# Kernel optimization log

Measured on AMD Instinct MI355X. Metric: run time of the kernel, lower is better.

The kernel has to match this reference:

```python
import jax, jax.numpy as jnp
import numpy as np

MARGIN = 0.3
N, D = 8192, 128
NUM_CLASSES = 512


def setup_inputs() -> dict:
    key = jax.random.key(0)
    k1, k2 = jax.random.split(key)
    embeddings = jax.random.normal(k1, (N, D), dtype=jnp.float32)
    targets = jax.random.randint(k2, (N,), 0, NUM_CLASSES, dtype=jnp.int64)
    return {"embeddings": embeddings, "targets": targets}


def reference(embeddings, targets):
    x = embeddings.astype(jnp.float32)
    # pairwise squared-euclidean: ||xi||^2 + ||xj||^2 - 2 xi.xj, clamped then sqrt
    sq = jnp.sum(x * x, axis=1)  # [N]
    dist = sq[:, None] + sq[None, :] - 2.0 * (x @ x.T)
    dist = jnp.sqrt(jnp.clip(dist, 1e-12, None))  # [N, N]

    is_pos = targets[:, None] == targets[None, :]  # includes diagonal, as in torch code

    # batch-hard mining: per-row hardest positive (max) and hardest negative (min)
    dist_ap = jnp.max(jnp.where(is_pos, dist, -jnp.inf), axis=1)
    dist_an = jnp.min(jnp.where(is_pos, jnp.inf, dist), axis=1)

    # MarginRankingLoss(margin)(dist_an, dist_ap, y=1) = mean(relu(margin - (dist_an - dist_ap)))
    loss = jnp.mean(jax.nn.relu(dist_ap - dist_an + MARGIN))
    return loss
```

## Files before the change

### kernel.cpp

```cpp
#include <hip/hip_runtime.h>
#include <hip/hip_bf16.h>

#define N_ROWS 8192
#define DIM 128
#define MARGIN_F 0.3f

typedef __attribute__((ext_vector_type(8))) short short8;
typedef __attribute__((ext_vector_type(4))) float f32x4;
typedef __attribute__((ext_vector_type(4))) int int4v;

__global__ __launch_bounds__(256) void prep_kernel(
    const float* __restrict__ x, const int* __restrict__ tgt,
    unsigned short* __restrict__ xbA, unsigned short* __restrict__ xbB,
    float2* __restrict__ meta, int* __restrict__ apb, int* __restrict__ anb) {
  const int w = threadIdx.x >> 6, l = threadIdx.x & 63;
  const int row = blockIdx.x * 4 + w;
  float2 v = reinterpret_cast<const float2*>(x + (size_t)row * DIM)[l];
  __hip_bfloat16 b0 = __float2bfloat16(v.x);
  __hip_bfloat16 b1 = __float2bfloat16(v.y);
  __hip_bfloat16 a0 = __float2bfloat16(-2.f * v.x);
  __hip_bfloat16 a1 = __float2bfloat16(-2.f * v.y);
  ushort2 stB, stA;
  stB.x = *reinterpret_cast<unsigned short*>(&b0);
  stB.y = *reinterpret_cast<unsigned short*>(&b1);
  stA.x = *reinterpret_cast<unsigned short*>(&a0);
  stA.y = *reinterpret_cast<unsigned short*>(&a1);
  const int c16 = row >> 4, l15r = row & 15;
  const int unit = c16 * 256 + (l >> 4) * 64 + ((l >> 2) & 3) * 16 + l15r;
  reinterpret_cast<ushort2*>(xbB)[unit * 4 + (l & 3)] = stB;
  reinterpret_cast<ushort2*>(xbA)[unit * 4 + (l & 3)] = stA;

  float s = v.x * v.x + v.y * v.y;
  #pragma unroll
  for (int off = 32; off >= 1; off >>= 1) s += __shfl_xor(s, off);
  if (l == 0) {
    float2 m;
    m.x = s;
    m.y = __int_as_float(tgt[row]);
    meta[row] = m;
    apb[row] = 0x00000000;
    anb[row] = 0x7f800000;
  }
}

__global__ __launch_bounds__(256, 2) void gram_mine_kernel(
    const unsigned short* __restrict__ xbA, const unsigned short* __restrict__ xbB,
    const float2* __restrict__ meta, int* __restrict__ apb, int* __restrict__ anb) {
  const int t = threadIdx.x;
  const int w = t >> 6, l = t & 63;
  const int l15 = l & 15, l4 = l >> 4;
  const int rb = blockIdx.x * 128 + w * 32;
  const int chunk = blockIdx.y * 1024;
  const int chunkb = chunk >> 4;

  const short8* xfA = reinterpret_cast<const short8*>(xbA);
  const short8* xfB = reinterpret_cast<const short8*>(xbB);

  short8 a0[4], a1[4];
  #pragma unroll
  for (int kk = 0; kk < 4; ++kk) {
    a0[kk] = xfA[(rb >> 4) * 256 + kk * 64 + l];
    a1[kk] = xfA[((rb >> 4) + 1) * 256 + kk * 64 + l];
  }

  int t_r[8];
  #pragma unroll
  for (int rf = 0; rf < 2; ++rf)
    #pragma unroll
    for (int rg = 0; rg < 4; ++rg)
      t_r[rf * 4 + rg] = __float_as_int(meta[rb + rf * 16 + l4 * 4 + rg].y);

  float ap2[8], an2[8];
  #pragma unroll
  for (int i = 0; i < 8; ++i) { ap2[i] = -__builtin_inff(); an2[i] = __builtin_inff(); }

  short8 bb0[8], bb1[8];
  float2 mc0[2], mc1[2];
  f32x4 accA[2][2], accB[2][2];

#define PREF_B(IDX, BB) do {                                                  \
    const int cb16_ = chunkb + (IDX) * 2;                                     \
    _Pragma("unroll")                                                         \
    for (int kk_ = 0; kk_ < 4; ++kk_) {                                       \
      BB[kk_ * 2 + 0] = xfB[(cb16_ + 0) * 256 + kk_ * 64 + l];                \
      BB[kk_ * 2 + 1] = xfB[(cb16_ + 1) * 256 + kk_ * 64 + l];                \
    } } while (0)

#define META_L(IDX, MC) do {                                                  \
    MC[0] = meta[chunk + (IDX) * 32 + l15];                                   \
    MC[1] = meta[chunk + (IDX) * 32 + 16 + l15];  } while (0)

#define MFMA_T(BB, MC, ACC) do {                                              \
    _Pragma("unroll")                                                         \
    for (int cf_ = 0; cf_ < 2; ++cf_) {                                       \
      float s_ = MC[cf_].x;                                                   \
      f32x4 ci_ = {s_, s_, s_, s_};                                           \
      ACC[0][cf_] = ci_; ACC[1][cf_] = ci_;                                   \
    }                                                                         \
    _Pragma("unroll")                                                         \
    for (int kk_ = 0; kk_ < 4; ++kk_) {                                       \
      _Pragma("unroll")                                                       \
      for (int cf_ = 0; cf_ < 2; ++cf_) {                                     \
        ACC[0][cf_] = __builtin_amdgcn_mfma_f32_16x16x32_bf16(                \
            a0[kk_], BB[kk_ * 2 + cf_], ACC[0][cf_], 0, 0, 0);                \
        ACC[1][cf_] = __builtin_amdgcn_mfma_f32_16x16x32_bf16(                \
            a1[kk_], BB[kk_ * 2 + cf_], ACC[1][cf_], 0, 0, 0);                \
      } } } while (0)

#define EPI_T(ACC, MC) do {                                                   \
    _Pragma("unroll")                                                         \
    for (int cf_ = 0; cf_ < 2; ++cf_) {                                       \
      const int tc_ = __float_as_int(MC[cf_].y);                              \
      _Pragma("unroll")                                                       \
      for (int rf_ = 0; rf_ < 2; ++rf_) {                                     \
        _Pragma("unroll")                                                     \
        for (int rg_ = 0; rg_ < 4; ++rg_) {                                   \
          const int ix_ = rf_ * 4 + rg_;                                      \
          float v_ = ACC[rf_][cf_][rg_];                                      \
          bool p_ = (t_r[ix_] == tc_);                                        \
          ap2[ix_] = p_ ? fmaxf(ap2[ix_], v_) : ap2[ix_];                     \
          an2[ix_] = p_ ? an2[ix_] : fminf(an2[ix_], v_);                     \
        } } } } while (0)

  PREF_B(0, bb0); META_L(0, mc0);
  MFMA_T(bb0, mc0, accA); PREF_B(1, bb1); META_L(1, mc1);

  #pragma unroll 1
  for (int p = 0; p < 15; ++p) {
    const int o = 2 * p + 1;
    MFMA_T(bb1, mc1, accB); PREF_B(o + 1, bb0); EPI_T(accA, mc0); META_L(o + 1, mc0);
    MFMA_T(bb0, mc0, accA); PREF_B(o + 2, bb1); EPI_T(accB, mc1); META_L(o + 2, mc1);
  }
  MFMA_T(bb1, mc1, accB); EPI_T(accA, mc0); EPI_T(accB, mc1);

#undef PREF_B
#undef META_L
#undef MFMA_T
#undef EPI_T

  #pragma unroll
  for (int i = 0; i < 8; ++i) {
    #pragma unroll
    for (int off = 1; off < 16; off <<= 1) {
      ap2[i] = fmaxf(ap2[i], __shfl_xor(ap2[i], off));
      an2[i] = fminf(an2[i], __shfl_xor(an2[i], off));
    }
  }
  if (l15 == 0) {
    #pragma unroll
    for (int rf = 0; rf < 2; ++rf)
      #pragma unroll
      for (int rg = 0; rg < 4; ++rg) {
        int row = rb + rf * 16 + l4 * 4 + rg;
        float sqr = meta[row].x;
        float a2 = fmaxf(ap2[rf * 4 + rg] + sqr, 1e-12f);
        float n2 = fmaxf(an2[rf * 4 + rg] + sqr, 1e-12f);
        atomicMax(apb + row, __float_as_int(a2));
        atomicMin(anb + row, __float_as_int(n2));
      }
  }
}

__global__ __launch_bounds__(1024) void loss_kernel(
    const int4v* __restrict__ apb, const int4v* __restrict__ anb,
    float* __restrict__ out) {
  __shared__ float red[16];
  float s = 0.f;
  for (int i = threadIdx.x; i < N_ROWS / 4; i += 1024) {
    int4v a4 = apb[i], n4 = anb[i];
    #pragma unroll
    for (int j = 0; j < 4; ++j) {
      float ap = sqrtf(__int_as_float(a4[j]));
      float an = sqrtf(__int_as_float(n4[j]));
      float li = ap - an + MARGIN_F;
      s += li > 0.f ? li : 0.f;
    }
  }
  #pragma unroll
  for (int off = 32; off >= 1; off >>= 1) s += __shfl_xor(s, off);
  const int w = threadIdx.x >> 6, l = threadIdx.x & 63;
  if (l == 0) red[w] = s;
  __syncthreads();
  if (threadIdx.x < 16) {
    float v = red[threadIdx.x];
    #pragma unroll
    for (int off = 8; off >= 1; off >>= 1) v += __shfl_xor(v, off);
    if (threadIdx.x == 0) out[0] = v / (float)N_ROWS;
  }
}

extern "C" void kernel_launch(void* const* d_in, const int* in_sizes, int n_in,
                              void* d_out, int out_size, void* d_ws, size_t ws_size,
                              hipStream_t stream) {
  const float* x = (const float*)d_in[0];
  const int* tgt = (const int*)d_in[1];
  float* out = (float*)d_out;

  char* ws = (char*)d_ws;
  unsigned short* xbA = (unsigned short*)ws;
  unsigned short* xbB = (unsigned short*)(ws + 2097152);
  float2* meta = (float2*)(ws + 4194304);
  int* apb = (int*)(ws + 4194304 + 65536);
  int* anb = (int*)(ws + 4194304 + 65536 + 32768);

  prep_kernel<<<2048, 256, 0, stream>>>(x, tgt, xbA, xbB, meta, apb, anb);
  gram_mine_kernel<<<dim3(64, 8), 256, 0, stream>>>(xbA, xbB, meta, apb, anb);
  loss_kernel<<<1, 1024, 0, stream>>>((const int4v*)apb, (const int4v*)anb, out);
}
```

Measured before the change: 44.28 us.

## Sort rows by class to skip positive-mask checks on disjoint tiles

Adds histogram and scatter kernels that counting-sort rows by target class. Embeddings are then laid out in class order, and each tile checks whether its row and column class ranges overlap. Tiles with disjoint ranges use a cheap min-only epilogue and skip the per-element class compare and max/min selects. This costs two extra kernel launches, one of which is a single-block scan, plus indirect row gathers and scattered atomics.

```diff
diff --git a/kernel.cpp b/kernel.cpp
--- a/kernel.cpp
+++ b/kernel.cpp
@@ -3,19 +3,54 @@
 
 #define N_ROWS 8192
 #define DIM 128
+#define NUM_CLS 512
 #define MARGIN_F 0.3f
 
 typedef __attribute__((ext_vector_type(8))) short short8;
 typedef __attribute__((ext_vector_type(4))) float f32x4;
 typedef __attribute__((ext_vector_type(4))) int int4v;
 
+__global__ __launch_bounds__(512) void hist_kernel(
+    const int* __restrict__ tgt, int* __restrict__ class_start,
+    int* __restrict__ cnt) {
+  __shared__ int h[NUM_CLS];
+  const int t = threadIdx.x;
+  h[t] = 0;
+  cnt[t] = 0;
+  __syncthreads();
+  for (int i = t; i < N_ROWS; i += 512) atomicAdd(&h[tgt[i]], 1);
+  __syncthreads();
+  int own = h[t];
+  int incl = own;
+  for (int off = 1; off < NUM_CLS; off <<= 1) {
+    int v = (t >= off) ? h[t - off] : 0;
+    __syncthreads();
+    incl += v;
+    h[t] = incl;
+    __syncthreads();
+  }
+  class_start[t] = incl - own;
+}
+
+__global__ __launch_bounds__(256) void scatter_kernel(
+    const int* __restrict__ tgt, const int* __restrict__ class_start,
+    int* __restrict__ cnt, int* __restrict__ sorted_row, int* __restrict__ cls) {
+  const int i = blockIdx.x * 256 + threadIdx.x;
+  const int c = tgt[i];
+  const int pos = class_start[c] + atomicAdd(&cnt[c], 1);
+  sorted_row[pos] = i;
+  cls[pos] = c;
+}
+
 __global__ __launch_bounds__(256) void prep_kernel(
-    const float* __restrict__ x, const int* __restrict__ tgt,
-    unsigned short* __restrict__ xbA, unsigned short* __restrict__ xbB,
-    float2* __restrict__ meta, int* __restrict__ apb, int* __restrict__ anb) {
+    const float* __restrict__ x, const int* __restrict__ sorted_row,
+    const int* __restrict__ cls, unsigned short* __restrict__ xbA,
+    unsigned short* __restrict__ xbB, float2* __restrict__ meta,
+    int* __restrict__ apb, int* __restrict__ anb) {
   const int w = threadIdx.x >> 6, l = threadIdx.x & 63;
-  const int row = blockIdx.x * 4 + w;
-  float2 v = reinterpret_cast<const float2*>(x + (size_t)row * DIM)[l];
+  const int j = blockIdx.x * 4 + w;
+  const int r = sorted_row[j];
+  float2 v = reinterpret_cast<const float2*>(x + (size_t)r * DIM)[l];
   __hip_bfloat16 b0 = __float2bfloat16(v.x);
   __hip_bfloat16 b1 = __float2bfloat16(v.y);
   __hip_bfloat16 a0 = __float2bfloat16(-2.f * v.x);
@@ -25,7 +60,7 @@
   stB.y = *reinterpret_cast<unsigned short*>(&b1);
   stA.x = *reinterpret_cast<unsigned short*>(&a0);
   stA.y = *reinterpret_cast<unsigned short*>(&a1);
-  const int c16 = row >> 4, l15r = row & 15;
+  const int c16 = j >> 4, l15r = j & 15;
   const int unit = c16 * 256 + (l >> 4) * 64 + ((l >> 2) & 3) * 16 + l15r;
   reinterpret_cast<ushort2*>(xbB)[unit * 4 + (l & 3)] = stB;
   reinterpret_cast<ushort2*>(xbA)[unit * 4 + (l & 3)] = stA;
@@ -36,16 +71,17 @@
   if (l == 0) {
     float2 m;
     m.x = s;
-    m.y = __int_as_float(tgt[row]);
-    meta[row] = m;
-    apb[row] = 0x00000000;
-    anb[row] = 0x7f800000;
+    m.y = __int_as_float(cls[j]);
+    meta[j] = m;
+    apb[r] = 0x00000000;
+    anb[r] = 0x7f800000;
   }
 }
 
 __global__ __launch_bounds__(256, 2) void gram_mine_kernel(
     const unsigned short* __restrict__ xbA, const unsigned short* __restrict__ xbB,
-    const float2* __restrict__ meta, int* __restrict__ apb, int* __restrict__ anb) {
+    const float2* __restrict__ meta, const int* __restrict__ cls,
+    const int* __restrict__ sorted_row, int* __restrict__ apb, int* __restrict__ anb) {
   const int t = threadIdx.x;
   const int w = t >> 6, l = t & 63;
   const int l15 = l & 15, l4 = l >> 4;
@@ -63,6 +99,7 @@
     a1[kk] = xfA[((rb >> 4) + 1) * 256 + kk * 64 + l];
   }
 
+  const int rcl_lo = cls[rb], rcl_hi = cls[rb + 31];
   int t_r[8];
   #pragma unroll
   for (int rf = 0; rf < 2; ++rf)
@@ -76,6 +113,7 @@
 
   short8 bb0[8], bb1[8];
   float2 mc0[2], mc1[2];
+  int cl0a, cl0b, cl1a, cl1b;
   f32x4 accA[2][2], accB[2][2];
 
 #define PREF_B(IDX, BB) do {                                                  \
@@ -86,9 +124,11 @@
       BB[kk_ * 2 + 1] = xfB[(cb16_ + 1) * 256 + kk_ * 64 + l];                \
     } } while (0)
 
-#define META_L(IDX, MC) do {                                                  \
+#define META_L(IDX, MC, CLA, CLB) do {                                        \
     MC[0] = meta[chunk + (IDX) * 32 + l15];                                   \
-    MC[1] = meta[chunk + (IDX) * 32 + 16 + l15];  } while (0)
+    MC[1] = meta[chunk + (IDX) * 32 + 16 + l15];                              \
+    CLA = cls[chunk + (IDX) * 32];                                            \
+    CLB = cls[chunk + (IDX) * 32 + 31]; } while (0)
 
 #define MFMA_T(BB, MC, ACC) do {                                              \
     _Pragma("unroll")                                                         \
@@ -107,31 +147,47 @@
             a1[kk_], BB[kk_ * 2 + cf_], ACC[1][cf_], 0, 0, 0);                \
       } } } while (0)
 
-#define EPI_T(ACC, MC) do {                                                   \
-    _Pragma("unroll")                                                         \
-    for (int cf_ = 0; cf_ < 2; ++cf_) {                                       \
-      const int tc_ = __float_as_int(MC[cf_].y);                              \
+#define EPI_T(ACC, MC, CLA, CLB) do {                                         \
+    if ((CLB) < rcl_lo || (CLA) > rcl_hi) {                                   \
+                               \
       _Pragma("unroll")                                                       \
       for (int rf_ = 0; rf_ < 2; ++rf_) {                                     \
         _Pragma("unroll")                                                     \
         for (int rg_ = 0; rg_ < 4; ++rg_) {                                   \
           const int ix_ = rf_ * 4 + rg_;                                      \
-          float v_ = ACC[rf_][cf_][rg_];                                      \
-          bool p_ = (t_r[ix_] == tc_);                                        \
-          ap2[ix_] = p_ ? fmaxf(ap2[ix_], v_) : ap2[ix_];                     \
-          an2[ix_] = p_ ? an2[ix_] : fminf(an2[ix_], v_);                     \
-        } } } } while (0)
-
-  PREF_B(0, bb0); META_L(0, mc0);
-  MFMA_T(bb0, mc0, accA); PREF_B(1, bb1); META_L(1, mc1);
+          an2[ix_] = fminf(fminf(ACC[rf_][0][rg_], ACC[rf_][1][rg_]),         \
+                           an2[ix_]);                                         \
+        } }                                                                   \
+    } else {                                                                  \
+      _Pragma("unroll")                                                       \
+      for (int cf_ = 0; cf_ < 2; ++cf_) {                                     \
+        const int tc_ = __float_as_int(MC[cf_].y);                            \
+        _Pragma("unroll")                                                     \
+        for (int rf_ = 0; rf_ < 2; ++rf_) {                                   \
+          _Pragma("unroll")                                                   \
+          for (int rg_ = 0; rg_ < 4; ++rg_) {                                 \
+            const int ix_ = rf_ * 4 + rg_;                                    \
+            float v_ = ACC[rf_][cf_][rg_];                                    \
+            bool p_ = (t_r[ix_] == tc_);                                      \
+            ap2[ix_] = p_ ? fmaxf(ap2[ix_], v_) : ap2[ix_];                   \
+            an2[ix_] = p_ ? an2[ix_] : fminf(an2[ix_], v_);                   \
+          } } }                                                               \
+    } } while (0)
+
+  PREF_B(0, bb0); META_L(0, mc0, cl0a, cl0b);
+  MFMA_T(bb0, mc0, accA); PREF_B(1, bb1); META_L(1, mc1, cl1a, cl1b);
 
   #pragma unroll 1
   for (int p = 0; p < 15; ++p) {
     const int o = 2 * p + 1;
-    MFMA_T(bb1, mc1, accB); PREF_B(o + 1, bb0); EPI_T(accA, mc0); META_L(o + 1, mc0);
-    MFMA_T(bb0, mc0, accA); PREF_B(o + 2, bb1); EPI_T(accB, mc1); META_L(o + 2, mc1);
-  }
-  MFMA_T(bb1, mc1, accB); EPI_T(accA, mc0); EPI_T(accB, mc1);
+    MFMA_T(bb1, mc1, accB); PREF_B(o + 1, bb0);
+    EPI_T(accA, mc0, cl0a, cl0b); META_L(o + 1, mc0, cl0a, cl0b);
+    MFMA_T(bb0, mc0, accA); PREF_B(o + 2, bb1);
+    EPI_T(accB, mc1, cl1a, cl1b); META_L(o + 2, mc1, cl1a, cl1b);
+  }
+  MFMA_T(bb1, mc1, accB);
+  EPI_T(accA, mc0, cl0a, cl0b);
+  EPI_T(accB, mc1, cl1a, cl1b);
 
 #undef PREF_B
 #undef META_L
@@ -152,11 +208,12 @@
       #pragma unroll
       for (int rg = 0; rg < 4; ++rg) {
         int row = rb + rf * 16 + l4 * 4 + rg;
+        int ro = sorted_row[row];
         float sqr = meta[row].x;
         float a2 = fmaxf(ap2[rf * 4 + rg] + sqr, 1e-12f);
         float n2 = fmaxf(an2[rf * 4 + rg] + sqr, 1e-12f);
-        atomicMax(apb + row, __float_as_int(a2));
-        atomicMin(anb + row, __float_as_int(n2));
+        atomicMax(apb + ro, __float_as_int(a2));
+        atomicMin(anb + ro, __float_as_int(n2));
       }
   }
 }
@@ -200,10 +257,17 @@
   unsigned short* xbA = (unsigned short*)ws;
   unsigned short* xbB = (unsigned short*)(ws + 2097152);
   float2* meta = (float2*)(ws + 4194304);
-  int* apb = (int*)(ws + 4194304 + 65536);
-  int* anb = (int*)(ws + 4194304 + 65536 + 32768);
-
-  prep_kernel<<<2048, 256, 0, stream>>>(x, tgt, xbA, xbB, meta, apb, anb);
-  gram_mine_kernel<<<dim3(64, 8), 256, 0, stream>>>(xbA, xbB, meta, apb, anb);
+  int* apb = (int*)(ws + 4259840);
+  int* anb = (int*)(ws + 4292608);
+  int* sorted_row = (int*)(ws + 4325376);
+  int* cls = (int*)(ws + 4358144);
+  int* class_start = (int*)(ws + 4390912);
+  int* cnt = (int*)(ws + 4392960);
+
+  hist_kernel<<<1, 512, 0, stream>>>(tgt, class_start, cnt);
+  scatter_kernel<<<32, 256, 0, stream>>>(tgt, class_start, cnt, sorted_row, cls);
+  prep_kernel<<<2048, 256, 0, stream>>>(x, sorted_row, cls, xbA, xbB, meta, apb, anb);
+  gram_mine_kernel<<<dim3(64, 8), 256, 0, stream>>>(xbA, xbB, meta, cls,
+                                                    sorted_row, apb, anb);
   loss_kernel<<<1, 1024, 0, stream>>>((const int4v*)apb, (const int4v*)anb, out);
 }
```

Measured after the change: 50.67 us. 14.4% more time.

## Stage B tiles in LDS via async global_load_lds with XOR swizzle

Applied to the files above, without the earlier changes.

Before, every wave fetched B fragments straight from global memory into registers. Now B is stored row-major by the prep kernel, and each block cooperatively stages 64-column slices into a 4-buffer LDS ring using direct global-to-LDS loads, with an XOR swizzle to avoid bank conflicts. Blocks grow to 512 threads (8 waves) sharing each B tile, and the grid changes to 32x16. This cuts redundant global and L2 traffic for B, at the cost of barriers per slice, 64KB of LDS per block, and a smaller in-register accumulator pipeline.

```diff
diff --git a/kernel.cpp b/kernel.cpp
--- a/kernel.cpp
+++ b/kernel.cpp
@@ -9,9 +9,16 @@
 typedef __attribute__((ext_vector_type(4))) float f32x4;
 typedef __attribute__((ext_vector_type(4))) int int4v;
 
+typedef const void __attribute__((address_space(1)))* gas1_t;
+typedef void __attribute__((address_space(3)))* las3_t;
+
+__device__ __forceinline__ void load_lds16(const void* g, void* l) {
+  __builtin_amdgcn_global_load_lds((gas1_t)g, (las3_t)l, 16, 0, 0);
+}
+
 __global__ __launch_bounds__(256) void prep_kernel(
     const float* __restrict__ x, const int* __restrict__ tgt,
-    unsigned short* __restrict__ xbA, unsigned short* __restrict__ xbB,
+    unsigned short* __restrict__ xbA, unsigned short* __restrict__ xbBrow,
     float2* __restrict__ meta, int* __restrict__ apb, int* __restrict__ anb) {
   const int w = threadIdx.x >> 6, l = threadIdx.x & 63;
   const int row = blockIdx.x * 4 + w;
@@ -25,9 +32,9 @@
   stB.y = *reinterpret_cast<unsigned short*>(&b1);
   stA.x = *reinterpret_cast<unsigned short*>(&a0);
   stA.y = *reinterpret_cast<unsigned short*>(&a1);
+  reinterpret_cast<ushort2*>(xbBrow)[(size_t)row * 64 + l] = stB;
   const int c16 = row >> 4, l15r = row & 15;
   const int unit = c16 * 256 + (l >> 4) * 64 + ((l >> 2) & 3) * 16 + l15r;
-  reinterpret_cast<ushort2*>(xbB)[unit * 4 + (l & 3)] = stB;
   reinterpret_cast<ushort2*>(xbA)[unit * 4 + (l & 3)] = stA;
 
   float s = v.x * v.x + v.y * v.y;
@@ -43,18 +50,18 @@
   }
 }
 
-__global__ __launch_bounds__(256, 2) void gram_mine_kernel(
-    const unsigned short* __restrict__ xbA, const unsigned short* __restrict__ xbB,
+__global__ __launch_bounds__(512, 4) void gram_mine_kernel(
+    const unsigned short* __restrict__ xbA, const unsigned short* __restrict__ xbBrow,
     const float2* __restrict__ meta, int* __restrict__ apb, int* __restrict__ anb) {
+  __shared__ unsigned short Bs[4][64 * 128];
+
   const int t = threadIdx.x;
   const int w = t >> 6, l = t & 63;
   const int l15 = l & 15, l4 = l >> 4;
-  const int rb = blockIdx.x * 128 + w * 32;
-  const int chunk = blockIdx.y * 1024;
-  const int chunkb = chunk >> 4;
+  const int rb = blockIdx.x * 256 + w * 32;
+  const int chunk = blockIdx.y * 512;
 
   const short8* xfA = reinterpret_cast<const short8*>(xbA);
-  const short8* xfB = reinterpret_cast<const short8*>(xbB);
 
   short8 a0[4], a1[4];
   #pragma unroll
@@ -74,69 +81,77 @@
   #pragma unroll
   for (int i = 0; i < 8; ++i) { ap2[i] = -__builtin_inff(); an2[i] = __builtin_inff(); }
 
-  short8 bb0[8], bb1[8];
-  float2 mc0[2], mc1[2];
-  f32x4 accA[2][2], accB[2][2];
-
-#define PREF_B(IDX, BB) do {                                                  \
-    const int cb16_ = chunkb + (IDX) * 2;                                     \
-    _Pragma("unroll")                                                         \
-    for (int kk_ = 0; kk_ < 4; ++kk_) {                                       \
-      BB[kk_ * 2 + 0] = xfB[(cb16_ + 0) * 256 + kk_ * 64 + l];                \
-      BB[kk_ * 2 + 1] = xfB[(cb16_ + 1) * 256 + kk_ * 64 + l];                \
+#define STAGE(BUF, S) do {                                                    \
+    const int colbase_ = chunk + (S) * 64;                                    \
+    _Pragma("unroll")                                                         \
+    for (int r_ = 0; r_ < 2; ++r_) {                                          \
+      int c_ = r_ * 512 + t;                                                  \
+      int col_ = c_ >> 4;                                                     \
+      int off_ = ((c_ & 15) * 16) ^ ((col_ & 7) << 4);                        \
+      const char* src_ = reinterpret_cast<const char*>(xbBrow) +              \
+                         (size_t)(colbase_ + col_) * 256 + off_;              \
+      load_lds16(src_, (char*)(&Bs[BUF][0]) + c_ * 16);                       \
     } } while (0)
 
-#define META_L(IDX, MC) do {                                                  \
-    MC[0] = meta[chunk + (IDX) * 32 + l15];                                   \
-    MC[1] = meta[chunk + (IDX) * 32 + 16 + l15];  } while (0)
-
-#define MFMA_T(BB, MC, ACC) do {                                              \
-    _Pragma("unroll")                                                         \
-    for (int cf_ = 0; cf_ < 2; ++cf_) {                                       \
-      float s_ = MC[cf_].x;                                                   \
-      f32x4 ci_ = {s_, s_, s_, s_};                                           \
-      ACC[0][cf_] = ci_; ACC[1][cf_] = ci_;                                   \
-    }                                                                         \
+#define SLICE(S, VM) do {                                                     \
+    if ((S) + 2 < 8) STAGE(((S) + 2) & 3, (S) + 2);                           \
+    __builtin_amdgcn_sched_barrier(0);                                        \
+    asm volatile("s_waitcnt vmcnt(" #VM ")" ::: "memory");                    \
+    __builtin_amdgcn_s_barrier();                                             \
+    __builtin_amdgcn_sched_barrier(0);                                        \
+    float2 mc_[4];                                                            \
+    _Pragma("unroll")                                                         \
+    for (int cf_ = 0; cf_ < 4; ++cf_)                                         \
+      mc_[cf_] = meta[chunk + (S) * 64 + cf_ * 16 + l15];                     \
+    f32x4 acc_[2][4];                                                         \
+    _Pragma("unroll")                                                         \
+    for (int rf_ = 0; rf_ < 2; ++rf_)                                         \
+      _Pragma("unroll")                                                       \
+      for (int cf_ = 0; cf_ < 4; ++cf_)                                       \
+        acc_[rf_][cf_] = (f32x4){0.f, 0.f, 0.f, 0.f};                         \
+    __builtin_amdgcn_s_setprio(1);                                            \
     _Pragma("unroll")                                                         \
     for (int kk_ = 0; kk_ < 4; ++kk_) {                                       \
       _Pragma("unroll")                                                       \
-      for (int cf_ = 0; cf_ < 2; ++cf_) {                                     \
-        ACC[0][cf_] = __builtin_amdgcn_mfma_f32_16x16x32_bf16(                \
-            a0[kk_], BB[kk_ * 2 + cf_], ACC[0][cf_], 0, 0, 0);                \
-        ACC[1][cf_] = __builtin_amdgcn_mfma_f32_16x16x32_bf16(                \
-            a1[kk_], BB[kk_ * 2 + cf_], ACC[1][cf_], 0, 0, 0);                \
-      } } } while (0)
-
-#define EPI_T(ACC, MC) do {                                                   \
-    _Pragma("unroll")                                                         \
-    for (int cf_ = 0; cf_ < 2; ++cf_) {                                       \
-      const int tc_ = __float_as_int(MC[cf_].y);                              \
+      for (int cf_ = 0; cf_ < 4; ++cf_) {                                     \
+        int col_ = cf_ * 16 + l15;                                            \
+        int kb_ = (kk_ * 64 + l4 * 16) ^ ((col_ & 7) << 4);                   \
+        short8 b_ = *reinterpret_cast<const short8*>(                         \
+            reinterpret_cast<const char*>(&Bs[(S) & 3][0]) + col_ * 256 + kb_); \
+        acc_[0][cf_] = __builtin_amdgcn_mfma_f32_16x16x32_bf16(               \
+            a0[kk_], b_, acc_[0][cf_], 0, 0, 0);                              \
+        acc_[1][cf_] = __builtin_amdgcn_mfma_f32_16x16x32_bf16(               \
+            a1[kk_], b_, acc_[1][cf_], 0, 0, 0);                              \
+      } }                                                                     \
+    __builtin_amdgcn_s_setprio(0);                                            \
+    _Pragma("unroll")                                                         \
+    for (int cf_ = 0; cf_ < 4; ++cf_) {                                       \
+      const float sqc_ = mc_[cf_].x;                                          \
+      const int tc_ = __float_as_int(mc_[cf_].y);                             \
       _Pragma("unroll")                                                       \
-      for (int rf_ = 0; rf_ < 2; ++rf_) {                                     \
+      for (int rf_ = 0; rf_ < 2; ++rf_)                                       \
         _Pragma("unroll")                                                     \
         for (int rg_ = 0; rg_ < 4; ++rg_) {                                   \
           const int ix_ = rf_ * 4 + rg_;                                      \
-          float v_ = ACC[rf_][cf_][rg_];                                      \
+          float v_ = acc_[rf_][cf_][rg_] + sqc_;               \
           bool p_ = (t_r[ix_] == tc_);                                        \
           ap2[ix_] = p_ ? fmaxf(ap2[ix_], v_) : ap2[ix_];                     \
           an2[ix_] = p_ ? an2[ix_] : fminf(an2[ix_], v_);                     \
-        } } } } while (0)
-
-  PREF_B(0, bb0); META_L(0, mc0);
-  MFMA_T(bb0, mc0, accA); PREF_B(1, bb1); META_L(1, mc1);
-
-  #pragma unroll 1
-  for (int p = 0; p < 15; ++p) {
-    const int o = 2 * p + 1;
-    MFMA_T(bb1, mc1, accB); PREF_B(o + 1, bb0); EPI_T(accA, mc0); META_L(o + 1, mc0);
-    MFMA_T(bb0, mc0, accA); PREF_B(o + 2, bb1); EPI_T(accB, mc1); META_L(o + 2, mc1);
-  }
-  MFMA_T(bb1, mc1, accB); EPI_T(accA, mc0); EPI_T(accB, mc1);
-
-#undef PREF_B
-#undef META_L
-#undef MFMA_T
-#undef EPI_T
+        } } } while (0)
+
+  STAGE(0, 0);
+  STAGE(1, 1);
+  SLICE(0, 4);
+  SLICE(1, 4);
+  SLICE(2, 4);
+  SLICE(3, 4);
+  SLICE(4, 4);
+  SLICE(5, 4);
+  SLICE(6, 2);
+  SLICE(7, 0);
+
+#undef STAGE
+#undef SLICE
 
   #pragma unroll
   for (int i = 0; i < 8; ++i) {
@@ -198,12 +213,12 @@
 
   char* ws = (char*)d_ws;
   unsigned short* xbA = (unsigned short*)ws;
-  unsigned short* xbB = (unsigned short*)(ws + 2097152);
+  unsigned short* xbBrow = (unsigned short*)(ws + 2097152);
   float2* meta = (float2*)(ws + 4194304);
   int* apb = (int*)(ws + 4194304 + 65536);
   int* anb = (int*)(ws + 4194304 + 65536 + 32768);
 
-  prep_kernel<<<2048, 256, 0, stream>>>(x, tgt, xbA, xbB, meta, apb, anb);
-  gram_mine_kernel<<<dim3(64, 8), 256, 0, stream>>>(xbA, xbB, meta, apb, anb);
+  prep_kernel<<<2048, 256, 0, stream>>>(x, tgt, xbA, xbBrow, meta, apb, anb);
+  gram_mine_kernel<<<dim3(32, 16), 512, 0, stream>>>(xbA, xbBrow, meta, apb, anb);
   loss_kernel<<<1, 1024, 0, stream>>>((const int4v*)apb, (const int4v*)anb, out);
 }
```

Measured after the change: 45.28 us. 1.02x slower.

## Deepen B prefetch to four buffers, halve column chunks, add MFMA priority

Applied to the files above, without the earlier changes.

The gram/mining kernel now uses four register buffers for B tiles and metadata, prefetching three tiles ahead instead of one, so global load latency is better hidden behind MFMA work. The column chunk per block is halved to 512, which doubles the grid to 64x16 blocks and raises parallelism across CUs at the cost of twice as many atomic updates per row. s_setprio is raised around the MFMA sequence so matrix issue is favored over other waves' epilogue work. The extra buffers raise register pressure, which could lower occupancy under the (256,2) launch bounds.

```diff
diff --git a/kernel.cpp b/kernel.cpp
--- a/kernel.cpp
+++ b/kernel.cpp
@@ -50,7 +50,7 @@
   const int w = t >> 6, l = t & 63;
   const int l15 = l & 15, l4 = l >> 4;
   const int rb = blockIdx.x * 128 + w * 32;
-  const int chunk = blockIdx.y * 1024;
+  const int chunk = blockIdx.y * 512;
   const int chunkb = chunk >> 4;
 
   const short8* xfA = reinterpret_cast<const short8*>(xbA);
@@ -74,21 +74,19 @@
   #pragma unroll
   for (int i = 0; i < 8; ++i) { ap2[i] = -__builtin_inff(); an2[i] = __builtin_inff(); }
 
-  short8 bb0[8], bb1[8];
-  float2 mc0[2], mc1[2];
+  short8 b0[8], b1[8], b2[8], b3[8];
+  float2 m0[2], m1[2], m2[2], m3[2];
   f32x4 accA[2][2], accB[2][2];
 
-#define PREF_B(IDX, BB) do {                                                  \
+#define PREF(IDX, BB, MC) do {                                                \
     const int cb16_ = chunkb + (IDX) * 2;                                     \
     _Pragma("unroll")                                                         \
     for (int kk_ = 0; kk_ < 4; ++kk_) {                                       \
       BB[kk_ * 2 + 0] = xfB[(cb16_ + 0) * 256 + kk_ * 64 + l];                \
       BB[kk_ * 2 + 1] = xfB[(cb16_ + 1) * 256 + kk_ * 64 + l];                \
-    } } while (0)
-
-#define META_L(IDX, MC) do {                                                  \
+    }                                                                         \
     MC[0] = meta[chunk + (IDX) * 32 + l15];                                   \
-    MC[1] = meta[chunk + (IDX) * 32 + 16 + l15];  } while (0)
+    MC[1] = meta[chunk + (IDX) * 32 + 16 + l15]; } while (0)
 
 #define MFMA_T(BB, MC, ACC) do {                                              \
     _Pragma("unroll")                                                         \
@@ -97,6 +95,7 @@
       f32x4 ci_ = {s_, s_, s_, s_};                                           \
       ACC[0][cf_] = ci_; ACC[1][cf_] = ci_;                                   \
     }                                                                         \
+    __builtin_amdgcn_s_setprio(1);                                            \
     _Pragma("unroll")                                                         \
     for (int kk_ = 0; kk_ < 4; ++kk_) {                                       \
       _Pragma("unroll")                                                       \
@@ -105,7 +104,8 @@
             a0[kk_], BB[kk_ * 2 + cf_], ACC[0][cf_], 0, 0, 0);                \
         ACC[1][cf_] = __builtin_amdgcn_mfma_f32_16x16x32_bf16(                \
             a1[kk_], BB[kk_ * 2 + cf_], ACC[1][cf_], 0, 0, 0);                \
-      } } } while (0)
+      } }                                                                     \
+    __builtin_amdgcn_s_setprio(0); } while (0)
 
 #define EPI_T(ACC, MC) do {                                                   \
     _Pragma("unroll")                                                         \
@@ -122,19 +122,24 @@
           an2[ix_] = p_ ? an2[ix_] : fminf(an2[ix_], v_);                     \
         } } } } while (0)
 
-  PREF_B(0, bb0); META_L(0, mc0);
-  MFMA_T(bb0, mc0, accA); PREF_B(1, bb1); META_L(1, mc1);
+  PREF(0, b0, m0);
+  PREF(1, b1, m1);
+  PREF(2, b2, m2); MFMA_T(b0, m0, accA);
+  PREF(3, b3, m3); MFMA_T(b1, m1, accB); EPI_T(accA, m0);
 
   #pragma unroll 1
-  for (int p = 0; p < 15; ++p) {
-    const int o = 2 * p + 1;
-    MFMA_T(bb1, mc1, accB); PREF_B(o + 1, bb0); EPI_T(accA, mc0); META_L(o + 1, mc0);
-    MFMA_T(bb0, mc0, accA); PREF_B(o + 2, bb1); EPI_T(accB, mc1); META_L(o + 2, mc1);
-  }
-  MFMA_T(bb1, mc1, accB); EPI_T(accA, mc0); EPI_T(accB, mc1);
-
-#undef PREF_B
-#undef META_L
+  for (int q = 0; q < 3; ++q) {
+    const int tb = 4 * q + 2;
+    PREF(tb + 2, b0, m0); MFMA_T(b2, m2, accA); EPI_T(accB, m1);
+    PREF(tb + 3, b1, m1); MFMA_T(b3, m3, accB); EPI_T(accA, m2);
+    PREF(tb + 4, b2, m2); MFMA_T(b0, m0, accA); EPI_T(accB, m3);
+    PREF(tb + 5, b3, m3); MFMA_T(b1, m1, accB); EPI_T(accA, m0);
+  }
+  MFMA_T(b2, m2, accA); EPI_T(accB, m1);
+  MFMA_T(b3, m3, accB); EPI_T(accA, m2);
+  EPI_T(accB, m3);
+
+#undef PREF
 #undef MFMA_T
 #undef EPI_T
 
@@ -204,6 +209,6 @@
   int* anb = (int*)(ws + 4194304 + 65536 + 32768);
 
   prep_kernel<<<2048, 256, 0, stream>>>(x, tgt, xbA, xbB, meta, apb, anb);
-  gram_mine_kernel<<<dim3(64, 8), 256, 0, stream>>>(xbA, xbB, meta, apb, anb);
+  gram_mine_kernel<<<dim3(64, 16), 256, 0, stream>>>(xbA, xbB, meta, apb, anb);
   loss_kernel<<<1, 1024, 0, stream>>>((const int4v*)apb, (const int4v*)anb, out);
 }
```

After: 47.90 us. +8.2%, slower.
